# Kernel tuning notes

Measured on AMD Instinct MI355X. Metric: run time of the kernel, lower is better.

The kernel has to match this reference:

```python
import jax, jax.numpy as jnp
import numpy as np

N_NODES = 50000
N_EDGES = 150000
N_TRIS = 100000
F = 256
L = 4


def setup_inputs() -> dict:
    key = jax.random.key(0)
    ks = jax.random.split(key, 8)
    x = jax.random.normal(ks[0], (N_EDGES, F), dtype=jnp.float32)
    edge_nodes = jax.random.randint(ks[1], (N_EDGES, 2), 0, N_NODES)
    tri_edges = jax.random.randint(ks[2], (N_TRIS, 3), 0, N_EDGES)
    tri_signs = (jax.random.randint(ks[3], (N_TRIS, 3), 0, 2) * 2 - 1).astype(jnp.int32)
    std = float(np.sqrt(2.0 / (F + F)))  # xavier_uniform-equivalent std
    W0_stack = jax.random.normal(ks[4], (L, F, F), dtype=jnp.float32) * std
    W1_stack = jax.random.normal(ks[5], (L, F, F), dtype=jnp.float32) * std
    W2_stack = jax.random.normal(ks[6], (L, F, F), dtype=jnp.float32) * std
    W0_L = jax.random.normal(ks[7], (F, 1), dtype=jnp.float32) * float(np.sqrt(2.0 / (F + 1)))
    return {"x": x, "W0_stack": W0_stack, "W1_stack": W1_stack, "W2_stack": W2_stack,
            "W0_L": W0_L, "edge_nodes": edge_nodes, "tri_edges": tri_edges, "tri_signs": tri_signs}


def _b1_mm(edge_nodes, y):
    # B1 @ y : [E,F] -> [N,F];  B1[u,e] = -1, B1[v,e] = +1
    u, v = edge_nodes[:, 0], edge_nodes[:, 1]
    out = jnp.zeros((N_NODES, y.shape[1]), y.dtype)
    return out.at[u].add(-y).at[v].add(y)


def _b1t_mm(edge_nodes, z):
    # B1.T @ z : [N,F] -> [E,F]
    return z[edge_nodes[:, 1]] - z[edge_nodes[:, 0]]


def _b2t_mm(tri_edges, signs, y):
    # B2.T @ y : [E,F] -> [T,F]
    return jnp.einsum('tkf,tk->tf', y[tri_edges], signs)


def _b2_mm(tri_edges, signs, w):
    # B2 @ w : [T,F] -> [E,F]
    contrib = w[:, None, :] * signs[:, :, None]  # [T,3,F]
    out = jnp.zeros((N_EDGES, w.shape[1]), w.dtype)
    return out.at[tri_edges.reshape(-1)].add(contrib.reshape(-1, w.shape[1]))


def reference(x, W0_stack, W1_stack, W2_stack, W0_L, edge_nodes, tri_edges, tri_signs):
    signs = tri_signs.astype(x.dtype)
    for i in range(L):
        d2 = _b2_mm(tri_edges, signs, _b2t_mm(tri_edges, signs, x @ W2_stack[i]))
        d1 = x @ W1_stack[i]
        d0 = _b1t_mm(edge_nodes, _b1_mm(edge_nodes, x @ W0_stack[i]))
        x = jax.nn.relu(d2 + d1 + d0)
    return _b1_mm(edge_nodes, x @ W0_L)  # [N_NODES, 1]
```

## Files before the change

### kernel.cpp

```cpp
#include <hip/hip_runtime.h>

#define M_EDGES 150000
#define NN_NODES 50000
#define N_TRIS  100000
#define F 256
#define NLAYERS 4

#define T1 391
#define T2 782
#define TZW (T1 + T2)
#define ZW_PAD 1176
#define TPXZW 147
#define T0_64 2344
#define TPX64 293

typedef __attribute__((ext_vector_type(8))) __bf16 bf16x8;
typedef __attribute__((ext_vector_type(4))) float f32x4;

__device__ inline unsigned short f2bf(float f) {
    unsigned int u = __float_as_uint(f);
    u += 0x7fff + ((u >> 16) & 1);
    return (unsigned short)(u >> 16);
}
__device__ inline float bf2f(unsigned short h) {
    return __uint_as_float(((unsigned int)h) << 16);
}

__device__ inline void async16(const void* g, void* l) {
    __builtin_amdgcn_global_load_lds(
        (const __attribute__((address_space(1))) void*)g,
        (__attribute__((address_space(3))) void*)l, 16, 0, 0);
}


__global__ __launch_bounds__(512) void gemm_zw(
    const unsigned short* __restrict__ sb,
    const unsigned short* __restrict__ qb,
    const unsigned short* __restrict__ wt,
    unsigned short* __restrict__ zb,
    unsigned short* __restrict__ wb)
{
    __shared__ unsigned short As[128 * 32];
    __shared__ unsigned short Bs[256 * 32];

    const int b    = blockIdx.x;
    const int tile = (b & 7) * TPXZW + (b >> 3);
    if (tile >= TZW) return;

    int seg, tloc;
    if (tile < T1) { seg = 1; tloc = tile; }
    else           { seg = 2; tloc = tile - T1; }
    const unsigned short* Asrc = (seg == 1) ? sb : qb;
    const int nrows = (seg == 1) ? NN_NODES : N_TRIS;
    const unsigned short* wsel = wt + seg * 65536;
    unsigned short* dst = (seg == 1) ? zb : wb;

    const int tid  = threadIdx.x;
    const int bm0  = tloc * 128;
    const int wid  = tid >> 6;
    const int lane = tid & 63;
    const int lm   = lane & 15;
    const int lh   = lane >> 4;
    const int wm   = wid >> 2;
    const int wn   = wid & 3;
    const int wbase = tid & ~63;

    f32x4 cacc[4][4];
#pragma unroll
    for (int i = 0; i < 4; i++)
#pragma unroll
        for (int j = 0; j < 4; j++) cacc[i][j] = (f32x4){0.f, 0.f, 0.f, 0.f};

    for (int k0 = 0; k0 < 256; k0 += 32) {
        {
            int row = tid >> 2;
            int g   = (tid & 3) ^ ((row >> 1) & 3);
            int gr  = bm0 + row;
            if (gr > nrows - 1) gr = nrows - 1;
            async16(Asrc + (size_t)gr * 256 + k0 + g * 8,
                    As + (size_t)wbase * 8);
        }
#pragma unroll
        for (int ss = 0; ss < 2; ss++) {
            int i   = ss * 512 + tid;
            int row = i >> 2;
            int g   = (i & 3) ^ ((row >> 1) & 3);
            async16(wsel + (size_t)row * 256 + k0 + g * 8,
                    Bs + (size_t)(ss * 512 + wbase) * 8);
        }
        asm volatile("s_waitcnt vmcnt(0)" ::: "memory");
        __syncthreads();

        bf16x8 a[4], bfr[4];
#pragma unroll
        for (int i = 0; i < 4; i++) {
            int rr = wm * 64 + i * 16 + lm;
            a[i] = *(const bf16x8*)(As + rr * 32 + ((lh ^ ((rr >> 1) & 3)) * 8));
        }
#pragma unroll
        for (int j = 0; j < 4; j++) {
            int rr = wn * 64 + j * 16 + lm;
            bfr[j] = *(const bf16x8*)(Bs + rr * 32 + ((lh ^ ((rr >> 1) & 3)) * 8));
        }
#pragma unroll
        for (int i = 0; i < 4; i++)
#pragma unroll
            for (int j = 0; j < 4; j++)
                cacc[i][j] = __builtin_amdgcn_mfma_f32_16x16x32_bf16(
                    bfr[j], a[i], cacc[i][j], 0, 0, 0);
        __syncthreads();
    }

#pragma unroll
    for (int i = 0; i < 4; i++) {
        int grow = bm0 + wm * 64 + i * 16 + lm;
        if (grow < nrows) {
#pragma unroll
            for (int j = 0; j < 4; j++) {
                int col = wn * 64 + j * 16 + lh * 4;
                ushort4 r;
                r.x = f2bf(cacc[i][j][0]);
                r.y = f2bf(cacc[i][j][1]);
                r.z = f2bf(cacc[i][j][2]);
                r.w = f2bf(cacc[i][j][3]);
                *(ushort4*)(dst + (size_t)grow * 256 + col) = r;
            }
        }
    }
}

__global__ __launch_bounds__(256) void gemm_y1_relu(
    unsigned short* __restrict__ xb,
    const unsigned short* __restrict__ wt,
    const unsigned short* __restrict__ wb,
    const unsigned short* __restrict__ zb,
    const int* __restrict__ en,
    const int* __restrict__ eoff,
    const int* __restrict__ eadj,
    const float* __restrict__ wl,
    float* __restrict__ p,
    int last)
{
    __shared__ __align__(16) unsigned short smem[64 * 256];
    unsigned short* const As = smem;
    unsigned short* const Bs = smem + 64 * 32;

    const int b    = blockIdx.x;
    const int tile = (b & 7) * TPX64 + (b >> 3);

    const int tid  = threadIdx.x;
    const int bm0  = tile * 64;
    const int wid  = tid >> 6;
    const int lane = tid & 63;
    const int lm   = lane & 15;
    const int lh   = lane >> 4;
    const int wn   = wid;
    const int wbase = tid & ~63;

    f32x4 cacc[4][4];
#pragma unroll
    for (int i = 0; i < 4; i++)
#pragma unroll
        for (int j = 0; j < 4; j++) cacc[i][j] = (f32x4){0.f, 0.f, 0.f, 0.f};

    for (int k0 = 0; k0 < 256; k0 += 32) {
        {
            int row = tid >> 2;
            int g   = (tid & 3) ^ ((row >> 1) & 3);
            int gr  = bm0 + row;
            if (gr > M_EDGES - 1) gr = M_EDGES - 1;
            async16(xb + (size_t)gr * 256 + k0 + g * 8,
                    As + (size_t)wbase * 8);
        }
#pragma unroll
        for (int ss = 0; ss < 4; ss++) {
            int i   = ss * 256 + tid;
            int row = i >> 2;
            int g   = (i & 3) ^ ((row >> 1) & 3);
            async16(wt + (size_t)row * 256 + k0 + g * 8,
                    Bs + (size_t)(ss * 256 + wbase) * 8);
        }
        asm volatile("s_waitcnt vmcnt(0)" ::: "memory");
        __syncthreads();

        bf16x8 a[4], bfr[4];
#pragma unroll
        for (int i = 0; i < 4; i++) {
            int rr = i * 16 + lm;
            a[i] = *(const bf16x8*)(As + rr * 32 + ((lh ^ ((rr >> 1) & 3)) * 8));
        }
#pragma unroll
        for (int j = 0; j < 4; j++) {
            int rr = wn * 64 + j * 16 + lm;
            bfr[j] = *(const bf16x8*)(Bs + rr * 32 + ((lh ^ ((rr >> 1) & 3)) * 8));
        }
#pragma unroll
        for (int i = 0; i < 4; i++)
#pragma unroll
            for (int j = 0; j < 4; j++)
                cacc[i][j] = __builtin_amdgcn_mfma_f32_16x16x32_bf16(
                    bfr[j], a[i], cacc[i][j], 0, 0, 0);
        __syncthreads();
    }

#pragma unroll
    for (int i = 0; i < 4; i++) {
        int lr  = i * 16 + lm;
        int key = (lr & 7) << 4;
#pragma unroll
        for (int j = 0; j < 4; j++) {
            int colb = wn * 128 + j * 32 + lh * 8;
            ushort4 r;
            r.x = f2bf(cacc[i][j][0]);
            r.y = f2bf(cacc[i][j][1]);
            r.z = f2bf(cacc[i][j][2]);
            r.w = f2bf(cacc[i][j][3]);
            *(ushort4*)((char*)smem + (size_t)lr * 512 + (colb ^ key)) = r;
        }
    }
    __syncthreads();

    const int f = lane * 4;
    for (int k = 0; k < 8; k++) {
        int lr0 = k * 8 + wid;
        int lr1 = lr0 + 4;
        int e0  = bm0 + lr0;
        if (e0 >= M_EDGES) break;
        int e1  = bm0 + lr1;
        int ok1 = (e1 < M_EDGES);
        int e1c = ok1 ? e1 : (M_EDGES - 1);

        ushort4 yv0 = *(const ushort4*)((const char*)smem + (size_t)lr0 * 512 +
                                        ((lane * 8) ^ ((lr0 & 7) << 4)));
        ushort4 yv1 = *(const ushort4*)((const char*)smem + (size_t)lr1 * 512 +
                                        ((lane * 8) ^ ((lr1 & 7) << 4)));
        int u0 = en[2 * e0], v0 = en[2 * e0 + 1];
        int u1 = en[2 * e1c], v1 = en[2 * e1c + 1];
        ushort4 zv0 = *(const ushort4*)(zb + (size_t)v0 * 256 + f);
        ushort4 zu0 = *(const ushort4*)(zb + (size_t)u0 * 256 + f);
        ushort4 zv1 = *(const ushort4*)(zb + (size_t)v1 * 256 + f);
        ushort4 zu1 = *(const ushort4*)(zb + (size_t)u1 * 256 + f);
        int beg0 = eoff[e0], end0 = eoff[e0 + 1];
        int beg1 = eoff[e1c], end1 = eoff[e1c + 1];

        float s0x = bf2f(yv0.x) + bf2f(zv0.x) - bf2f(zu0.x);
        float s0y = bf2f(yv0.y) + bf2f(zv0.y) - bf2f(zu0.y);
        float s0z = bf2f(yv0.z) + bf2f(zv0.z) - bf2f(zu0.z);
        float s0w = bf2f(yv0.w) + bf2f(zv0.w) - bf2f(zu0.w);
        float s1x = bf2f(yv1.x) + bf2f(zv1.x) - bf2f(zu1.x);
        float s1y = bf2f(yv1.y) + bf2f(zv1.y) - bf2f(zu1.y);
        float s1z = bf2f(yv1.z) + bf2f(zv1.z) - bf2f(zu1.z);
        float s1w = bf2f(yv1.w) + bf2f(zv1.w) - bf2f(zu1.w);

        for (int i2 = beg0; i2 < end0; i2++) {
            int ta = eadj[i2];
            float sa = (ta & 1) ? -1.f : 1.f;
            ushort4 wa = *(const ushort4*)(wb + (size_t)(ta >> 1) * 256 + f);
            s0x += sa * bf2f(wa.x);
            s0y += sa * bf2f(wa.y);
            s0z += sa * bf2f(wa.z);
            s0w += sa * bf2f(wa.w);
        }
        for (int i2 = beg1; i2 < end1; i2++) {
            int ta = eadj[i2];
            float sa = (ta & 1) ? -1.f : 1.f;
            ushort4 wa = *(const ushort4*)(wb + (size_t)(ta >> 1) * 256 + f);
            s1x += sa * bf2f(wa.x);
            s1y += sa * bf2f(wa.y);
            s1z += sa * bf2f(wa.z);
            s1w += sa * bf2f(wa.w);
        }

        s0x = fmaxf(s0x, 0.f); s0y = fmaxf(s0y, 0.f);
        s0z = fmaxf(s0z, 0.f); s0w = fmaxf(s0w, 0.f);
        s1x = fmaxf(s1x, 0.f); s1y = fmaxf(s1y, 0.f);
        s1z = fmaxf(s1z, 0.f); s1w = fmaxf(s1w, 0.f);

        if (!last) {
            ushort4 r0;
            r0.x = f2bf(s0x); r0.y = f2bf(s0y);
            r0.z = f2bf(s0z); r0.w = f2bf(s0w);
            *(ushort4*)(xb + (size_t)e0 * 256 + f) = r0;
            if (ok1) {
                ushort4 r1;
                r1.x = f2bf(s1x); r1.y = f2bf(s1y);
                r1.z = f2bf(s1z); r1.w = f2bf(s1w);
                *(ushort4*)(xb + (size_t)e1 * 256 + f) = r1;
            }
        } else {
            float4 wv = *(const float4*)(wl + f);
            float d0 = s0x * wv.x + s0y * wv.y + s0z * wv.z + s0w * wv.w;
            float d1 = s1x * wv.x + s1y * wv.y + s1z * wv.z + s1w * wv.w;
#pragma unroll
            for (int off = 32; off > 0; off >>= 1) {
                d0 += __shfl_down(d0, off, 64);
                d1 += __shfl_down(d1, off, 64);
            }
            if (lane == 0) {
                p[e0] = d0;
                if (ok1) p[e1] = d1;
            }
        }
    }
}

__global__ __launch_bounds__(256) void count_nodes(
    const int* __restrict__ en, int* __restrict__ cnt)
{
    int e = blockIdx.x * 256 + threadIdx.x;
    if (e < M_EDGES) {
        atomicAdd(&cnt[en[2 * e]], 1);
        atomicAdd(&cnt[en[2 * e + 1]], 1);
    }
}

__global__ __launch_bounds__(256) void count_tris(
    const int* __restrict__ te, int* __restrict__ cnt)
{
    int t = blockIdx.x * 256 + threadIdx.x;
    if (t < N_TRIS) {
#pragma unroll
        for (int k = 0; k < 3; k++) atomicAdd(&cnt[te[3 * t + k]], 1);
    }
}

__global__ __launch_bounds__(256) void scan_block(
    const int* __restrict__ cnt, int* __restrict__ off,
    int* __restrict__ partial, int n)
{
    __shared__ int s[256];
    int t = threadIdx.x;
    int gid = blockIdx.x * 256 + t;
    int v = (gid < n) ? cnt[gid] : 0;
    s[t] = v;
    __syncthreads();
    for (int o = 1; o < 256; o <<= 1) {
        int x = (t >= o) ? s[t - o] : 0;
        __syncthreads();
        s[t] += x;
        __syncthreads();
    }
    if (gid < n) off[gid] = s[t] - v;
    if (t == 255) partial[blockIdx.x] = s[255];
}

__global__ __launch_bounds__(1024) void scan_partial(int* __restrict__ partial, int nb)
{
    __shared__ int s[1024];
    int t = threadIdx.x;
    int v = (t < nb) ? partial[t] : 0;
    s[t] = v;
    __syncthreads();
    for (int o = 1; o < 1024; o <<= 1) {
        int x = (t >= o) ? s[t - o] : 0;
        __syncthreads();
        s[t] += x;
        __syncthreads();
    }
    if (t < nb) partial[t] = s[t] - v;
}

__global__ __launch_bounds__(256) void scan_add(
    int* __restrict__ off, int* __restrict__ cursor,
    const int* __restrict__ partial, int n, int total)
{
    int gid = blockIdx.x * 256 + threadIdx.x;
    if (gid == 0) off[n] = total;
    if (gid < n) {
        int o = off[gid] + partial[blockIdx.x];
        off[gid] = o;
        cursor[gid] = o;
    }
}

__global__ __launch_bounds__(256) void fill_nodes(
    const int* __restrict__ en, int* __restrict__ cursor, int* __restrict__ adj)
{
    int e = blockIdx.x * 256 + threadIdx.x;
    if (e < M_EDGES) {
        int u = en[2 * e], v = en[2 * e + 1];
        adj[atomicAdd(&cursor[u], 1)] = (e << 1);
        adj[atomicAdd(&cursor[v], 1)] = (e << 1) | 1;
    }
}

__global__ __launch_bounds__(256) void fill_tris(
    const int* __restrict__ te, const int* __restrict__ ts,
    int* __restrict__ cursor, int* __restrict__ adj)
{
    int t = blockIdx.x * 256 + threadIdx.x;
    if (t < N_TRIS) {
#pragma unroll
        for (int k = 0; k < 3; k++) {
            int e = te[3 * t + k];
            int neg = (ts[3 * t + k] < 0) ? 1 : 0;
            adj[atomicAdd(&cursor[e], 1)] = (t << 1) | neg;
        }
    }
}

#define ZN_BLOCKS (NN_NODES / 4)
#define WT_BLOCKS (N_TRIS / 4)

__global__ __launch_bounds__(256) void agg_fused(
    const unsigned short* __restrict__ xb,
    const int* __restrict__ noff,
    const int* __restrict__ nadj,
    unsigned short* __restrict__ sbuf,
    const int* __restrict__ te,
    const int* __restrict__ ts,
    unsigned short* __restrict__ qbuf)
{
    int lane = threadIdx.x & 63;
    int f = lane * 4;
    if (blockIdx.x < ZN_BLOCKS) {
        int n = blockIdx.x * 4 + (threadIdx.x >> 6);
        int beg = noff[n], end = noff[n + 1];
        int deg = end - beg;
        int cl = beg + lane;
        if (cl > 2 * M_EDGES - 1) cl = 2 * M_EDGES - 1;
        int entL = nadj[cl];
        int dmax = (deg < 64) ? deg : 64;
        float ax = 0.f, ay = 0.f, az = 0.f, aw = 0.f;
        int j = 0;
        for (; j + 1 < dmax; j += 2) {
            int ea = __shfl(entL, j, 64);
            int eb = __shfl(entL, j + 1, 64);
            float sa = (ea & 1) ? 1.f : -1.f;
            float sgb = (eb & 1) ? 1.f : -1.f;
            ushort4 va = *(const ushort4*)(xb + (size_t)(ea >> 1) * 256 + f);
            ushort4 vb = *(const ushort4*)(xb + (size_t)(eb >> 1) * 256 + f);
            ax += sa * bf2f(va.x) + sgb * bf2f(vb.x);
            ay += sa * bf2f(va.y) + sgb * bf2f(vb.y);
            az += sa * bf2f(va.z) + sgb * bf2f(vb.z);
            aw += sa * bf2f(va.w) + sgb * bf2f(vb.w);
        }
        if (j < dmax) {
            int ea = __shfl(entL, j, 64);
            float sa = (ea & 1) ? 1.f : -1.f;
            ushort4 va = *(const ushort4*)(xb + (size_t)(ea >> 1) * 256 + f);
            ax += sa * bf2f(va.x);
            ay += sa * bf2f(va.y);
            az += sa * bf2f(va.z);
            aw += sa * bf2f(va.w);
        }
        for (int i = beg + 64; i < end; i++) {
            int ea = nadj[i];
            float sa = (ea & 1) ? 1.f : -1.f;
            ushort4 va = *(const ushort4*)(xb + (size_t)(ea >> 1) * 256 + f);
            ax += sa * bf2f(va.x);
            ay += sa * bf2f(va.y);
            az += sa * bf2f(va.z);
            aw += sa * bf2f(va.w);
        }
        ushort4 r;
        r.x = f2bf(ax); r.y = f2bf(ay); r.z = f2bf(az); r.w = f2bf(aw);
        *(ushort4*)(sbuf + (size_t)n * 256 + f) = r;
    } else {
        int t = (blockIdx.x - ZN_BLOCKS) * 4 + (threadIdx.x >> 6);
        int e0 = te[3 * t + 0], e1 = te[3 * t + 1], e2 = te[3 * t + 2];
        float s0 = (float)ts[3 * t + 0];
        float s1 = (float)ts[3 * t + 1];
        float s2 = (float)ts[3 * t + 2];
        ushort4 a4 = *(const ushort4*)(xb + (size_t)e0 * 256 + f);
        ushort4 b4 = *(const ushort4*)(xb + (size_t)e1 * 256 + f);
        ushort4 d4 = *(const ushort4*)(xb + (size_t)e2 * 256 + f);
        ushort4 r;
        r.x = f2bf(s0 * bf2f(a4.x) + s1 * bf2f(b4.x) + s2 * bf2f(d4.x));
        r.y = f2bf(s0 * bf2f(a4.y) + s1 * bf2f(b4.y) + s2 * bf2f(d4.y));
        r.z = f2bf(s0 * bf2f(a4.z) + s1 * bf2f(b4.z) + s2 * bf2f(d4.z));
        r.w = f2bf(s0 * bf2f(a4.w) + s1 * bf2f(b4.w) + s2 * bf2f(d4.w));
        *(ushort4*)(qbuf + (size_t)t * 256 + f) = r;
    }
}

__global__ __launch_bounds__(256) void out_nodes(
    const float* __restrict__ p,
    const int* __restrict__ noff,
    const int* __restrict__ nadj,
    float* __restrict__ out)
{
    int n = blockIdx.x * 256 + threadIdx.x;
    if (n >= NN_NODES) return;
    int beg = noff[n], end = noff[n + 1];
    float s = 0.f;
    for (int i = beg; i < end; i++) {
        int ent = nadj[i];
        float sg = (ent & 1) ? 1.f : -1.f;
        s += sg * p[ent >> 1];
    }
    out[n] = s;
}

__global__ __launch_bounds__(256) void cvt_x(
    const float* __restrict__ x, unsigned short* __restrict__ xb)
{
    int idx = blockIdx.x * 256 + threadIdx.x;
    float4 v = *(const float4*)(x + (size_t)idx * 4);
    ushort4 r;
    r.x = f2bf(v.x); r.y = f2bf(v.y); r.z = f2bf(v.z); r.w = f2bf(v.w);
    *(ushort4*)(xb + (size_t)idx * 4) = r;
}

__global__ __launch_bounds__(256) void cvt_w(
    const float* __restrict__ W0, const float* __restrict__ W1,
    const float* __restrict__ W2, unsigned short* __restrict__ wt)
{
    int idx = blockIdx.x * 256 + threadIdx.x;
    int l = idx / (3 * 65536);
    int rem = idx - l * (3 * 65536);
    int seg = rem >> 16;
    int n = (rem >> 8) & 255;
    int k = rem & 255;
    const float* src = (seg == 0) ? W1 : (seg == 1) ? W0 : W2;
    wt[idx] = f2bf(src[(size_t)l * 65536 + k * 256 + n]);
}

extern "C" void kernel_launch(void* const* d_in, const int* in_sizes, int n_in,
                              void* d_out, int out_size, void* d_ws, size_t ws_size,
                              hipStream_t stream)
{
    const float* x0  = (const float*)d_in[0];
    const float* W0s = (const float*)d_in[1];
    const float* W1s = (const float*)d_in[2];
    const float* W2s = (const float*)d_in[3];
    const float* WL  = (const float*)d_in[4];
    const int*   en  = (const int*)d_in[5];
    const int*   te  = (const int*)d_in[6];
    const int*   ts  = (const int*)d_in[7];
    float* out = (float*)d_out;

    const size_t MF = (size_t)M_EDGES * F;
    unsigned short* xb = (unsigned short*)d_ws;
    unsigned short* y1 = xb + MF;
    unsigned short* sbuf = y1 + MF;
    unsigned short* qbuf = sbuf + (size_t)NN_NODES * 256;
    unsigned short* wt = qbuf + (size_t)N_TRIS * 256;
    unsigned short* wb = wt + (size_t)4 * 3 * 65536;
    unsigned short* zb = wb + (size_t)N_TRIS * 256;
    float* p = (float*)(zb + (size_t)NN_NODES * 256);
    int* noff = (int*)(p + M_EDGES);
    int* ncur = noff + (NN_NODES + 1);
    int* nadj = ncur + NN_NODES;
    int* eoff = nadj + 2 * M_EDGES;
    int* ecur = eoff + (M_EDGES + 1);
    int* eadj = ecur + M_EDGES;
    int* part = eadj + 3 * N_TRIS;

    cvt_w<<<(4 * 3 * 65536) / 256, 256, 0, stream>>>(W0s, W1s, W2s, wt);
    cvt_x<<<(int)(MF / 4 / 256), 256, 0, stream>>>(x0, xb);

    const int nbN = (NN_NODES + 255) / 256;
    const int nbE = (M_EDGES + 255) / 256;
    hipMemsetAsync(ncur, 0, NN_NODES * sizeof(int), stream);
    hipMemsetAsync(ecur, 0, M_EDGES * sizeof(int), stream);
    count_nodes<<<nbE, 256, 0, stream>>>(en, ncur);
    count_tris<<<(N_TRIS + 255) / 256, 256, 0, stream>>>(te, ecur);
    scan_block<<<nbN, 256, 0, stream>>>(ncur, noff, part, NN_NODES);
    scan_partial<<<1, 1024, 0, stream>>>(part, nbN);
    scan_add<<<nbN, 256, 0, stream>>>(noff, ncur, part, NN_NODES, 2 * M_EDGES);
    fill_nodes<<<nbE, 256, 0, stream>>>(en, ncur, nadj);
    scan_block<<<nbE, 256, 0, stream>>>(ecur, eoff, part, M_EDGES);
    scan_partial<<<1, 1024, 0, stream>>>(part, nbE);
    scan_add<<<nbE, 256, 0, stream>>>(eoff, ecur, part, M_EDGES, 3 * N_TRIS);
    fill_tris<<<(N_TRIS + 255) / 256, 256, 0, stream>>>(te, ts, ecur, eadj);

    for (int l = 0; l < NLAYERS; l++) {
        agg_fused<<<ZN_BLOCKS + WT_BLOCKS, 256, 0, stream>>>(
            xb, noff, nadj, sbuf, te, ts, qbuf);
        gemm_zw<<<ZW_PAD, 512, 0, stream>>>(
            sbuf, qbuf, wt + (size_t)l * 3 * 65536, zb, wb);
        gemm_y1_relu<<<T0_64, 256, 0, stream>>>(
            xb, wt + (size_t)l * 3 * 65536, wb, zb, en, eoff, eadj,
            WL, p, (l == NLAYERS - 1) ? 1 : 0);
    }

    out_nodes<<<(NN_NODES + 255) / 256, 256, 0, stream>>>(p, noff, nadj, out);
}
```

Measured before the change: 1.210 ms.

## Load GEMM MFMA operands directly from global memory instead of LDS staging

Both GEMM kernels stop staging A and B tiles in LDS with async global-to-LDS copies and barriers. Each lane now loads its bf16x8 MFMA fragments straight from global memory using precomputed row pointers, and the per-iteration syncthreads calls are gone. This removes LDS traffic and barrier stalls but gives up intra-block reuse: several waves now redundantly fetch the same A and weight rows through the caches, and the loads are strided rather than coalesced.

Result: slower. 1.596 ms (+31.9%).

```diff
diff --git a/kernel.cpp b/kernel.cpp
--- a/kernel.cpp
+++ b/kernel.cpp
@@ -26,12 +26,6 @@
     return __uint_as_float(((unsigned int)h) << 16);
 }
 
-__device__ inline void async16(const void* g, void* l) {
-    __builtin_amdgcn_global_load_lds(
-        (const __attribute__((address_space(1))) void*)g,
-        (__attribute__((address_space(3))) void*)l, 16, 0, 0);
-}
-
 
 __global__ __launch_bounds__(512) void gemm_zw(
     const unsigned short* __restrict__ sb,
@@ -40,9 +34,6 @@
     unsigned short* __restrict__ zb,
     unsigned short* __restrict__ wb)
 {
-    __shared__ unsigned short As[128 * 32];
-    __shared__ unsigned short Bs[256 * 32];
-
     const int b    = blockIdx.x;
     const int tile = (b & 7) * TPXZW + (b >> 3);
     if (tile >= TZW) return;
@@ -63,7 +54,18 @@
     const int lh   = lane >> 4;
     const int wm   = wid >> 2;
     const int wn   = wid & 3;
-    const int wbase = tid & ~63;
+
+    const unsigned short* arow[4];
+#pragma unroll
+    for (int i = 0; i < 4; i++) {
+        int gr = bm0 + wm * 64 + i * 16 + lm;
+        if (gr > nrows - 1) gr = nrows - 1;
+        arow[i] = Asrc + (size_t)gr * 256 + lh * 8;
+    }
+    const unsigned short* brow[4];
+#pragma unroll
+    for (int j = 0; j < 4; j++)
+        brow[j] = wsel + (size_t)(wn * 64 + j * 16 + lm) * 256 + lh * 8;
 
     f32x4 cacc[4][4];
 #pragma unroll
@@ -72,43 +74,19 @@
         for (int j = 0; j < 4; j++) cacc[i][j] = (f32x4){0.f, 0.f, 0.f, 0.f};
 
     for (int k0 = 0; k0 < 256; k0 += 32) {
-        {
-            int row = tid >> 2;
-            int g   = (tid & 3) ^ ((row >> 1) & 3);
-            int gr  = bm0 + row;
-            if (gr > nrows - 1) gr = nrows - 1;
-            async16(Asrc + (size_t)gr * 256 + k0 + g * 8,
-                    As + (size_t)wbase * 8);
-        }
-#pragma unroll
-        for (int ss = 0; ss < 2; ss++) {
-            int i   = ss * 512 + tid;
-            int row = i >> 2;
-            int g   = (i & 3) ^ ((row >> 1) & 3);
-            async16(wsel + (size_t)row * 256 + k0 + g * 8,
-                    Bs + (size_t)(ss * 512 + wbase) * 8);
-        }
-        asm volatile("s_waitcnt vmcnt(0)" ::: "memory");
-        __syncthreads();
-
         bf16x8 a[4], bfr[4];
 #pragma unroll
-        for (int i = 0; i < 4; i++) {
-            int rr = wm * 64 + i * 16 + lm;
-            a[i] = *(const bf16x8*)(As + rr * 32 + ((lh ^ ((rr >> 1) & 3)) * 8));
-        }
-#pragma unroll
-        for (int j = 0; j < 4; j++) {
-            int rr = wn * 64 + j * 16 + lm;
-            bfr[j] = *(const bf16x8*)(Bs + rr * 32 + ((lh ^ ((rr >> 1) & 3)) * 8));
-        }
+        for (int i = 0; i < 4; i++)
+            a[i] = *(const bf16x8*)(arow[i] + k0);
+#pragma unroll
+        for (int j = 0; j < 4; j++)
+            bfr[j] = *(const bf16x8*)(brow[j] + k0);
 #pragma unroll
         for (int i = 0; i < 4; i++)
 #pragma unroll
             for (int j = 0; j < 4; j++)
                 cacc[i][j] = __builtin_amdgcn_mfma_f32_16x16x32_bf16(
                     bfr[j], a[i], cacc[i][j], 0, 0, 0);
-        __syncthreads();
     }
 
 #pragma unroll
@@ -142,8 +120,6 @@
     int last)
 {
     __shared__ __align__(16) unsigned short smem[64 * 256];
-    unsigned short* const As = smem;
-    unsigned short* const Bs = smem + 64 * 32;
 
     const int b    = blockIdx.x;
     const int tile = (b & 7) * TPX64 + (b >> 3);
@@ -155,7 +131,18 @@
     const int lm   = lane & 15;
     const int lh   = lane >> 4;
     const int wn   = wid;
-    const int wbase = tid & ~63;
+
+    const unsigned short* arow[4];
+#pragma unroll
+    for (int i = 0; i < 4; i++) {
+        int gr = bm0 + i * 16 + lm;
+        if (gr > M_EDGES - 1) gr = M_EDGES - 1;
+        arow[i] = xb + (size_t)gr * 256 + lh * 8;
+    }
+    const unsigned short* brow[4];
+#pragma unroll
+    for (int j = 0; j < 4; j++)
+        brow[j] = wt + (size_t)(wn * 64 + j * 16 + lm) * 256 + lh * 8;
 
     f32x4 cacc[4][4];
 #pragma unroll
@@ -164,43 +151,19 @@
         for (int j = 0; j < 4; j++) cacc[i][j] = (f32x4){0.f, 0.f, 0.f, 0.f};
 
     for (int k0 = 0; k0 < 256; k0 += 32) {
-        {
-            int row = tid >> 2;
-            int g   = (tid & 3) ^ ((row >> 1) & 3);
-            int gr  = bm0 + row;
-            if (gr > M_EDGES - 1) gr = M_EDGES - 1;
-            async16(xb + (size_t)gr * 256 + k0 + g * 8,
-                    As + (size_t)wbase * 8);
-        }
-#pragma unroll
-        for (int ss = 0; ss < 4; ss++) {
-            int i   = ss * 256 + tid;
-            int row = i >> 2;
-            int g   = (i & 3) ^ ((row >> 1) & 3);
-            async16(wt + (size_t)row * 256 + k0 + g * 8,
-                    Bs + (size_t)(ss * 256 + wbase) * 8);
-        }
-        asm volatile("s_waitcnt vmcnt(0)" ::: "memory");
-        __syncthreads();
-
         bf16x8 a[4], bfr[4];
 #pragma unroll
-        for (int i = 0; i < 4; i++) {
-            int rr = i * 16 + lm;
-            a[i] = *(const bf16x8*)(As + rr * 32 + ((lh ^ ((rr >> 1) & 3)) * 8));
-        }
-#pragma unroll
-        for (int j = 0; j < 4; j++) {
-            int rr = wn * 64 + j * 16 + lm;
-            bfr[j] = *(const bf16x8*)(Bs + rr * 32 + ((lh ^ ((rr >> 1) & 3)) * 8));
-        }
+        for (int i = 0; i < 4; i++)
+            a[i] = *(const bf16x8*)(arow[i] + k0);
+#pragma unroll
+        for (int j = 0; j < 4; j++)
+            bfr[j] = *(const bf16x8*)(brow[j] + k0);
 #pragma unroll
         for (int i = 0; i < 4; i++)
 #pragma unroll
             for (int j = 0; j < 4; j++)
                 cacc[i][j] = __builtin_amdgcn_mfma_f32_16x16x32_bf16(
                     bfr[j], a[i], cacc[i][j], 0, 0, 0);
-        __syncthreads();
     }
 
 #pragma unroll
```
